# Kernel optimization log

Measured on AMD Instinct MI355X. Metric: run time of the kernel, lower is better.

The kernel has to match this reference:

```python
import jax, jax.numpy as jnp
import numpy as np

N = 65536   # total goals in library
D = 256     # flattened embedding dim
B = 2048    # batch_size (last B entries are the new batch)


def setup_inputs() -> dict:
    key = jax.random.key(0)
    k1, k2 = jax.random.split(key)
    return {
        "target_lib": jax.random.normal(k1, (N, D), dtype=jnp.float32),
        "reached_lib": jax.random.normal(k2, (N, D), dtype=jnp.float32),
        "batch_size": B,
    }


def _euclid(a, b):
    # distance_fn: Euclidean distance between two embeddings
    return jnp.sqrt(jnp.sum((a - b) ** 2))


def _nearest_idx(queries, lib):
    # top-1 nearest neighbor via squared-distance expansion (same argmin as cdist)
    qn = jnp.sum(queries * queries, axis=1, keepdims=True)      # [B,1]
    ln = jnp.sum(lib * lib, axis=1)                             # [L]
    d2 = qn + ln[None, :] - 2.0 * (queries @ lib.T)             # [B,L]
    return jnp.argmin(d2, axis=1)                               # [B]


def reference(target_lib, reached_lib, batch_size):
    targets = target_lib[-batch_size:]          # [B,D] newest target goals
    reached = reached_lib[-batch_size:]         # [B,D] newest reached goals
    prev = reached_lib[:-batch_size]            # [N-B,D] previously reached goals

    prev_closest = prev[_nearest_idx(targets, prev)]       # [B,D]
    new_closest = reached[_nearest_idx(targets, reached)]  # [B,D]

    def LP(t, init_e, reached_e):
        return _euclid(t, init_e) - _euclid(t, reached_e)

    IM_vals, IM_grads = jax.vmap(jax.value_and_grad(LP, 0))(
        targets, prev_closest, new_closest)
    return IM_vals, IM_grads
```

## Files before the change

kernel.cpp:

```cpp
#include <hip/hip_runtime.h>
#include <math.h>

#define NTOT   65536
#define DDIM   256
#define BATCH  2048
#define NPREV  (NTOT - BATCH)

#define PWP    32
#define PWR    32
#define UPC_P  31
#define UPC_R  1
#define BNC_P  31
#define BNC_R  16

#define INF_F 3.402823466e+38f
#define SWZ(r) ((((r) & 3)) ^ ((((r) >> 2) & 3)))

typedef float  f32x4  __attribute__((ext_vector_type(4)));
typedef float  f32x16 __attribute__((ext_vector_type(16)));
typedef _Float16 half8 __attribute__((ext_vector_type(8)));

#define TILE_HALVES 65536

#define SCHED_FENCE() __builtin_amdgcn_sched_barrier(0)
#define RAW_BARRIER() do { SCHED_FENCE(); __builtin_amdgcn_s_barrier(); SCHED_FENCE(); } while (0)
#define VMCNT2()  do { asm volatile("s_waitcnt vmcnt(2)" ::: "memory"); SCHED_FENCE(); } while (0)
#define VMCNT0()  do { asm volatile("s_waitcnt vmcnt(0)" ::: "memory"); SCHED_FENCE(); } while (0)
#define LGKM0()   do { asm volatile("s_waitcnt lgkmcnt(0)" ::: "memory"); SCHED_FENCE(); } while (0)

__global__ void lp_norms(const float* __restrict__ lib, float* __restrict__ ln) {
    const int row  = blockIdx.x * 4 + (threadIdx.x >> 6);
    const int lane = threadIdx.x & 63;
    const float4 v = reinterpret_cast<const float4*>(lib + (size_t)row * DDIM)[lane];
    float s = v.x * v.x + v.y * v.y + v.z * v.z + v.w * v.w;
#pragma unroll
    for (int off = 32; off > 0; off >>= 1) s += __shfl_down(s, off);
    if (lane == 0) ln[row] = s;
}

__device__ __forceinline__ void cvt_split(const f32x4 a, const f32x4 b,
                                          half8& h, half8& l) {
    float v[8] = {a[0], a[1], a[2], a[3], b[0], b[1], b[2], b[3]};
#pragma unroll
    for (int j = 0; j < 8; ++j) {
        const float s = v[j] * 256.0f;
        const _Float16 hh = (_Float16)s;
        const _Float16 ll = (_Float16)(s - (float)hh);
        h[j] = hh; l[j] = ll;
    }
}

__global__ void lp_split32(const float* __restrict__ src, _Float16* __restrict__ dst,
                           float* __restrict__ ln) {
    const int tile = blockIdx.x;
    const int t    = threadIdx.x;
    const int rg   = t >> 6;
    const int l    = t & 63;
    const int row  = rg * 32 + (l & 31);
    const int k8   = l >> 5;
    const float* srcR = src + (size_t)tile * 128 * DDIM + (size_t)row * DDIM;
    _Float16*    dstT = dst + (size_t)tile * TILE_HALVES;

    float nsum = 0.f;
#pragma unroll
    for (int kb = 0; kb < 8; ++kb) {
#pragma unroll
        for (int kk = 0; kk < 2; ++kk) {
            const float* p = srcR + kb * 32 + kk * 16 + k8 * 8;
            const f32x4 a = *reinterpret_cast<const f32x4*>(p);
            const f32x4 b = *reinterpret_cast<const f32x4*>(p + 4);
            half8 h, lo; cvt_split(a, b, h, lo);
            const size_t off = ((size_t)(((kb * 2 + 0) * 4 + rg) * 2 + kk) * 64 + l) * 8;
            *reinterpret_cast<half8*>(dstT + off)        = h;
            *reinterpret_cast<half8*>(dstT + off + 4096) = lo;
            nsum += a[0]*a[0] + a[1]*a[1] + a[2]*a[2] + a[3]*a[3]
                  + b[0]*b[0] + b[1]*b[1] + b[2]*b[2] + b[3]*b[3];
        }
    }
    nsum += __shfl_xor(nsum, 32);
    if (ln != nullptr && k8 == 0) ln[(size_t)tile * 128 + row] = nsum;
}

__device__ __forceinline__ void gload16(const _Float16* g, _Float16* lds) {
    __builtin_amdgcn_global_load_lds(
        (const __attribute__((address_space(1))) void*)g,
        (__attribute__((address_space(3))) void*)lds, 16, 0, 0);
}

#define NN_STEP(kb_, RC, RN, STAGE_OK, VM, READ_OK)                              \
  {                                                                              \
    const int s_ = un * 8 + (kb_);                                               \
    if (STAGE_OK) stageL((s_ + 2) % 3, s_ + 2);                                  \
    VM;                                                                          \
    RAW_BARRIER();                                                               \
    LGKM0();                                                                     \
    __builtin_amdgcn_s_setprio(1);                                               \
    _Pragma("unroll")                                                            \
    for (int kk = 0; kk < 2; ++kk)                                               \
      _Pragma("unroll")                                                          \
      for (int term = 0; term < 3; ++term) {                                     \
        const int ta = (term == 2) ? 1 : 0;                                      \
        const int tb = (term == 1) ? 1 : 0;                                      \
        acc[0] = __builtin_amdgcn_mfma_f32_32x32x16_f16(                         \
            qf[kb_][ta][kk], RC[0][tb][kk], acc[0], 0, 0, 0);                    \
        acc[1] = __builtin_amdgcn_mfma_f32_32x32x16_f16(                         \
            qf[kb_][ta][kk], RC[1][tb][kk], acc[1], 0, 0, 0);                    \
      }                                                                          \
    __builtin_amdgcn_s_setprio(0);                                               \
    if (READ_OK) {                                                               \
      const _Float16* Bn = &LB[(s_ + 1) % 3][0];                                 \
      _Pragma("unroll")                                                          \
      for (int nf = 0; nf < 2; ++nf)                                             \
        _Pragma("unroll")                                                        \
        for (int hl = 0; hl < 2; ++hl)                                           \
          _Pragma("unroll")                                                      \
          for (int kk = 0; kk < 2; ++kk)                                         \
            RN[nf][hl][kk] = *reinterpret_cast<const half8*>(                    \
                Bn + hl * 2048 + nf * 1024 + kk * 512 + lane * 8);               \
    }                                                                            \
  }

__global__ __launch_bounds__(256, 2)
void lp_nn_mfma10(const _Float16* __restrict__ Qs, const _Float16* __restrict__ Ls,
                  const float* __restrict__ ln, int unitsPC, int nchunks,
                  float* __restrict__ pscore, int* __restrict__ pidx)
{
    __shared__ _Float16 LB[3][4096];
    __shared__ float lnLds[2048];

    const int nwg  = 16 * nchunks;
    const int hid  = blockIdx.x;
    const int work = (hid & 7) * (nwg >> 3) + (hid >> 3);
    const int bx   = work & 15;
    const int by   = work >> 4;

    const int t    = threadIdx.x;
    const int lane = t & 63;
    const int wid  = t >> 6;
    const int col  = lane & 31, hi = lane >> 5;

    const _Float16* Qt = Qs + (size_t)bx * TILE_HALVES;
    const int u0    = by * unitsPC;
    const int NSTEP = unitsPC * 8;

    half8 qf[8][2][2];
#pragma unroll
    for (int kb = 0; kb < 8; ++kb)
#pragma unroll
        for (int hl = 0; hl < 2; ++hl)
#pragma unroll
            for (int kk = 0; kk < 2; ++kk)
                qf[kb][hl][kk] = *reinterpret_cast<const half8*>(
                    Qt + ((((kb * 2 + hl) * 4 + wid) * 2) + kk) * 512 + lane * 8);

    auto stageL = [&](int buf, int s) {
        const int u = u0 + (s >> 3), kb = s & 7;
        const int tile = u >> 1, half = u & 1;
        const _Float16* base = Ls + (size_t)tile * TILE_HALVES;
#pragma unroll
        for (int hl = 0; hl < 2; ++hl)
            gload16(base + ((kb * 2 + hl) * 4 + half * 2) * 1024 + t * 8,
                    &LB[buf][hl * 2048 + wid * 512]);
    };

    float bkey[16];
    int   bidxr[16];
    f32x16 acc[2];
#pragma unroll
    for (int r = 0; r < 16; ++r) { bkey[r] = INF_F; bidxr[r] = 0x7fffffff; }
    acc[0] = (f32x16)(0.f); acc[1] = (f32x16)(0.f);

    auto fold = [&](int un) {
        const int u = u0 + un;
        const float lnv0 = lnLds[un * 64 + col];
        const float lnv1 = lnLds[un * 64 + 32 + col];
#pragma unroll
        for (int nf = 0; nf < 2; ++nf) {
            const int gidx = u * 64 + nf * 32 + col;
            const float lnvs = (nf ? lnv1 : lnv0) * 65536.0f;
#pragma unroll
            for (int r = 0; r < 16; ++r) {
                const float key = fmaf(-2.f, acc[nf][r], lnvs);
                if (key < bkey[r] || (key == bkey[r] && gidx < bidxr[r])) {
                    bkey[r] = key; bidxr[r] = gidx;
                }
                acc[nf][r] = 0.f;
            }
        }
    };

    {
        const float* lsrc = ln + (size_t)u0 * 64;
#pragma unroll
        for (int j = 0; j < 2; ++j)
            __builtin_amdgcn_global_load_lds(
                (const __attribute__((address_space(1))) void*)(lsrc + j * 1024 + t * 4),
                (__attribute__((address_space(3))) void*)(&lnLds[j * 1024 + wid * 256]),
                16, 0, 0);
    }
    stageL(0, 0);
    stageL(1, 1);
    VMCNT2();
    RAW_BARRIER();

    half8 bfA[2][2][2], bfB[2][2][2];
#pragma unroll
    for (int nf = 0; nf < 2; ++nf)
#pragma unroll
        for (int hl = 0; hl < 2; ++hl)
#pragma unroll
            for (int kk = 0; kk < 2; ++kk)
                bfA[nf][hl][kk] = *reinterpret_cast<const half8*>(
                    &LB[0][0] + hl * 2048 + nf * 1024 + kk * 512 + lane * 8);

    for (int un = 0; un < unitsPC - 1; ++un) {
        NN_STEP(0, bfA, bfB, true, VMCNT2(), true)
        NN_STEP(1, bfB, bfA, true, VMCNT2(), true)
        NN_STEP(2, bfA, bfB, true, VMCNT2(), true)
        NN_STEP(3, bfB, bfA, true, VMCNT2(), true)
        NN_STEP(4, bfA, bfB, true, VMCNT2(), true)
        NN_STEP(5, bfB, bfA, true, VMCNT2(), true)
        NN_STEP(6, bfA, bfB, true, VMCNT2(), true)
        NN_STEP(7, bfB, bfA, true, VMCNT2(), true)
        fold(un);
    }
    {
        const int un = unitsPC - 1;
        NN_STEP(0, bfA, bfB, true,  VMCNT2(), true)
        NN_STEP(1, bfB, bfA, true,  VMCNT2(), true)
        NN_STEP(2, bfA, bfB, true,  VMCNT2(), true)
        NN_STEP(3, bfB, bfA, true,  VMCNT2(), true)
        NN_STEP(4, bfA, bfB, true,  VMCNT2(), true)
        NN_STEP(5, bfB, bfA, true,  VMCNT2(), true)
        NN_STEP(6, bfA, bfB, false, VMCNT0(), true)
        NN_STEP(7, bfB, bfA, false, VMCNT0(), false)
        fold(un);
    }

#pragma unroll
    for (int off = 1; off < 32; off <<= 1)
#pragma unroll
        for (int r = 0; r < 16; ++r) {
            const float ok = __shfl_xor(bkey[r], off);
            const int   oi = __shfl_xor(bidxr[r], off);
            if (ok < bkey[r] || (ok == bkey[r] && oi < bidxr[r])) {
                bkey[r] = ok; bidxr[r] = oi;
            }
        }
    if (col == 0)
#pragma unroll
        for (int r = 0; r < 16; ++r) {
            const int q = bx * 128 + wid * 32 + (r & 3) + 8 * (r >> 2) + 4 * hi;
            pscore[(size_t)q * nchunks + by] = bkey[r];
            pidx  [(size_t)q * nchunks + by] = bidxr[r];
        }
}

__global__ __launch_bounds__(256, 2)
void lp_nn_mfma_fb(const float* __restrict__ Q, const float* __restrict__ L,
                   const float* __restrict__ ln, int chunkRows,
                   float* __restrict__ pscore, int* __restrict__ pidx, int nchunks)
{
    __shared__ _Float16 Ah[128 * 32];
    __shared__ _Float16 Al[128 * 32];
    __shared__ _Float16 Bh[128 * 32];
    __shared__ _Float16 Bl[128 * 32];
    __shared__ float xk[2][128];
    __shared__ int   xi[2][128];

    const int t    = threadIdx.x;
    const int wid  = t >> 6, lane = t & 63;
    const int wq   = wid >> 1, wl = wid & 1;
    const int col  = lane & 15, rg = lane >> 4;
    const int qbase = blockIdx.x * 128;
    const int chunkBase = blockIdx.y * chunkRows;
    const int srow   = t >> 2;
    const int schunk = t & 3;

    float bkey[4][4];
    int   bidxr[4][4];
#pragma unroll
    for (int mf = 0; mf < 4; ++mf)
#pragma unroll
        for (int i = 0; i < 4; ++i) { bkey[mf][i] = INF_F; bidxr[mf][i] = 0x7fffffff; }

    for (int lt = 0; lt < chunkRows; lt += 128) {
        f32x4 acc[4][4];
#pragma unroll
        for (int mf = 0; mf < 4; ++mf)
#pragma unroll
            for (int nf = 0; nf < 4; ++nf) acc[mf][nf] = (f32x4)(0.f);

        for (int kb = 0; kb < DDIM; kb += 32) {
            __syncthreads();
#pragma unroll
            for (int sr = 0; sr < 2; ++sr) {
                const int r = srow + 64 * sr;
                const int s = schunk ^ SWZ(r);
                {
                    const float* src = Q + (size_t)(qbase + r) * DDIM + kb + schunk * 8;
                    const f32x4 a = *reinterpret_cast<const f32x4*>(src);
                    const f32x4 b = *reinterpret_cast<const f32x4*>(src + 4);
                    half8 h, l; cvt_split(a, b, h, l);
                    *reinterpret_cast<half8*>(&Ah[r * 32 + s * 8]) = h;
                    *reinterpret_cast<half8*>(&Al[r * 32 + s * 8]) = l;
                }
                {
                    const float* src = L + (size_t)(chunkBase + lt + r) * DDIM + kb + schunk * 8;
                    const f32x4 a = *reinterpret_cast<const f32x4*>(src);
                    const f32x4 b = *reinterpret_cast<const f32x4*>(src + 4);
                    half8 h, l; cvt_split(a, b, h, l);
                    *reinterpret_cast<half8*>(&Bh[r * 32 + s * 8]) = h;
                    *reinterpret_cast<half8*>(&Bl[r * 32 + s * 8]) = l;
                }
            }
            __syncthreads();

            half8 ah[4], al[4];
#pragma unroll
            for (int mf = 0; mf < 4; ++mf) {
                const int r = wq * 64 + mf * 16 + col;
                const int s = rg ^ SWZ(r);
                ah[mf] = *reinterpret_cast<const half8*>(&Ah[r * 32 + s * 8]);
                al[mf] = *reinterpret_cast<const half8*>(&Al[r * 32 + s * 8]);
            }
#pragma unroll
            for (int nf = 0; nf < 4; ++nf) {
                const int r = wl * 64 + nf * 16 + col;
                const int s = rg ^ SWZ(r);
                const half8 bh = *reinterpret_cast<const half8*>(&Bh[r * 32 + s * 8]);
                const half8 bl = *reinterpret_cast<const half8*>(&Bl[r * 32 + s * 8]);
#pragma unroll
                for (int mf = 0; mf < 4; ++mf) {
                    acc[mf][nf] = __builtin_amdgcn_mfma_f32_16x16x32_f16(ah[mf], bh, acc[mf][nf], 0, 0, 0);
                    acc[mf][nf] = __builtin_amdgcn_mfma_f32_16x16x32_f16(ah[mf], bl, acc[mf][nf], 0, 0, 0);
                    acc[mf][nf] = __builtin_amdgcn_mfma_f32_16x16x32_f16(al[mf], bh, acc[mf][nf], 0, 0, 0);
                }
            }
        }

#pragma unroll
        for (int nf = 0; nf < 4; ++nf) {
            const int gidx = chunkBase + lt + wl * 64 + nf * 16 + col;
            const float lnv = ln[gidx] * 65536.0f;
#pragma unroll
            for (int mf = 0; mf < 4; ++mf)
#pragma unroll
                for (int i = 0; i < 4; ++i) {
                    const float key = fmaf(-2.f, acc[mf][nf][i], lnv);
                    if (key < bkey[mf][i] || (key == bkey[mf][i] && gidx < bidxr[mf][i])) {
                        bkey[mf][i] = key; bidxr[mf][i] = gidx;
                    }
                }
        }
    }

#pragma unroll
    for (int off = 1; off < 16; off <<= 1)
#pragma unroll
        for (int mf = 0; mf < 4; ++mf)
#pragma unroll
            for (int i = 0; i < 4; ++i) {
                const float ok = __shfl_xor(bkey[mf][i], off);
                const int   oi = __shfl_xor(bidxr[mf][i], off);
                if (ok < bkey[mf][i] || (ok == bkey[mf][i] && oi < bidxr[mf][i])) {
                    bkey[mf][i] = ok; bidxr[mf][i] = oi;
                }
            }
    if (col == 0)
#pragma unroll
        for (int mf = 0; mf < 4; ++mf)
#pragma unroll
            for (int i = 0; i < 4; ++i) {
                const int ql = wq * 64 + mf * 16 + rg * 4 + i;
                xk[wl][ql] = bkey[mf][i];
                xi[wl][ql] = bidxr[mf][i];
            }
    __syncthreads();
    if (t < 128) {
        float bk = xk[0][t]; int bi = xi[0][t];
        const float k2 = xk[1][t]; const int i2 = xi[1][t];
        if (k2 < bk || (k2 == bk && i2 < bi)) { bk = k2; bi = i2; }
        const int q = qbase + t;
        pscore[(size_t)q * nchunks + blockIdx.y] = bk;
        pidx  [(size_t)q * nchunks + blockIdx.y] = bi;
    }
}

__global__ void lp_finalize(const float* __restrict__ Q,
                            const float* __restrict__ prevL,
                            const float* __restrict__ reachL,
                            const float* __restrict__ ps_p, const int* __restrict__ pi_p,
                            const float* __restrict__ ps_r, const int* __restrict__ pi_r,
                            int ncp, int ncr,
                            float* __restrict__ out)
{
    const int q = blockIdx.x;
    const int lane = threadIdx.x;

    float k1 = (lane < ncp) ? ps_p[(size_t)q * ncp + lane] : INF_F;
    int   i1 = (lane < ncp) ? pi_p[(size_t)q * ncp + lane] : 0x7fffffff;
#pragma unroll
    for (int off = 32; off > 0; off >>= 1) {
        const float ok = __shfl_xor(k1, off);
        const int   oi = __shfl_xor(i1, off);
        if (ok < k1 || (ok == k1 && oi < i1)) { k1 = ok; i1 = oi; }
    }
    float k2 = (lane < ncr) ? ps_r[(size_t)q * ncr + lane] : INF_F;
    int   i2 = (lane < ncr) ? pi_r[(size_t)q * ncr + lane] : 0x7fffffff;
#pragma unroll
    for (int off = 32; off > 0; off >>= 1) {
        const float ok = __shfl_xor(k2, off);
        const int   oi = __shfl_xor(i2, off);
        if (ok < k2 || (ok == k2 && oi < i2)) { k2 = ok; i2 = oi; }
    }

    const float4 tv = reinterpret_cast<const float4*>(Q      + (size_t)q  * DDIM)[lane];
    const float4 e1 = reinterpret_cast<const float4*>(prevL  + (size_t)i1 * DDIM)[lane];
    const float4 e2 = reinterpret_cast<const float4*>(reachL + (size_t)i2 * DDIM)[lane];
    const float4 d1 = {tv.x - e1.x, tv.y - e1.y, tv.z - e1.z, tv.w - e1.w};
    const float4 d2 = {tv.x - e2.x, tv.y - e2.y, tv.z - e2.z, tv.w - e2.w};
    float s1 = d1.x * d1.x + d1.y * d1.y + d1.z * d1.z + d1.w * d1.w;
    float s2 = d2.x * d2.x + d2.y * d2.y + d2.z * d2.z + d2.w * d2.w;
#pragma unroll
    for (int off = 32; off > 0; off >>= 1) {
        s1 += __shfl_xor(s1, off);
        s2 += __shfl_xor(s2, off);
    }
    const float r1 = sqrtf(s1), r2 = sqrtf(s2);
    float4 g;
    g.x = d1.x / r1 - d2.x / r2;
    g.y = d1.y / r1 - d2.y / r2;
    g.z = d1.z / r1 - d2.z / r2;
    g.w = d1.w / r1 - d2.w / r2;
    reinterpret_cast<float4*>(out + BATCH + (size_t)q * DDIM)[lane] = g;
    if (lane == 0) out[q] = r1 - r2;
}

extern "C" void kernel_launch(void* const* d_in, const int* in_sizes, int n_in,
                              void* d_out, int out_size, void* d_ws, size_t ws_size,
                              hipStream_t stream) {
    const float* target_lib  = (const float*)d_in[0];
    const float* reached_lib = (const float*)d_in[1];
    const float* Qp     = target_lib  + (size_t)NPREV * DDIM;
    const float* prevL  = reached_lib;
    const float* reachL = reached_lib + (size_t)NPREV * DDIM;

    float* ws     = (float*)d_ws;
    float* ln_all = ws;
    float* ps_p   = ln_all + NTOT;
    float* ps_r   = ps_p + (size_t)BATCH * PWP;
    int*   pi_p   = (int*)(ps_r + (size_t)BATCH * PWR);
    int*   pi_r   = pi_p + (size_t)BATCH * PWP;
    _Float16* Qsp = (_Float16*)(pi_r + (size_t)BATCH * PWR);
    _Float16* Lsp = Qsp + (size_t)(BATCH / 128) * TILE_HALVES;
    float* out    = (float*)d_out;

    const size_t need = (size_t)(NTOT + 2 * BATCH * (PWP + PWR)) * 4
                      + (size_t)(BATCH / 128 + NTOT / 128) * TILE_HALVES * 2;

    if (ws_size >= need) {
        lp_split32<<<NTOT / 128, 256, 0, stream>>>(reached_lib, Lsp, ln_all);
        lp_split32<<<BATCH / 128, 256, 0, stream>>>(Qp, Qsp, nullptr);
        lp_nn_mfma10<<<16 * PWP, 256, 0, stream>>>(
            Qsp, Lsp, ln_all, UPC_P, PWP, ps_p, pi_p);
        lp_nn_mfma10<<<16 * PWR, 256, 0, stream>>>(
            Qsp, Lsp + (size_t)(NPREV / 128) * TILE_HALVES,
            ln_all + NPREV, UPC_R, PWR, ps_r, pi_r);
        lp_finalize<<<BATCH, 64, 0, stream>>>(
            Qp, prevL, reachL, ps_p, pi_p, ps_r, pi_r, PWP, PWR, out);
    } else {
        lp_norms<<<NTOT / 4, 256, 0, stream>>>(reached_lib, ln_all);
        lp_nn_mfma_fb<<<dim3(BATCH / 128, BNC_P), 256, 0, stream>>>(
            Qp, prevL, ln_all, 2048, ps_p, pi_p, BNC_P);
        lp_nn_mfma_fb<<<dim3(BATCH / 128, BNC_R), 256, 0, stream>>>(
            Qp, reachL, ln_all + NPREV, 128, ps_r, pi_r, BNC_R);
        lp_finalize<<<BATCH, 64, 0, stream>>>(
            Qp, prevL, reachL, ps_p, pi_p, ps_r, pi_r, BNC_P, BNC_R, out);
    }
}
```

Before: 237.0 us.

## Stage two k-blocks per LDS buffer to halve barriers in NN MFMA loop

The nearest-neighbour MFMA kernel now stages two k-blocks of library fragments per triple-buffered LDS slot, with the LDS buffers doubled to match. Each pair of k-steps shares one wait and one barrier, and the next pair's loads are issued between the two MFMA groups. The aim is to halve the per-step barrier and waitcnt overhead. In exchange, each iteration waits for all outstanding global loads (vmcnt(0)), including the prefetch that was just issued. That shortens the effective prefetch distance and could expose memory latency. LDS use per block also grows.

```diff
diff --git a/kernel.cpp b/kernel.cpp
--- a/kernel.cpp
+++ b/kernel.cpp
@@ -24,7 +24,7 @@
 
 #define SCHED_FENCE() __builtin_amdgcn_sched_barrier(0)
 #define RAW_BARRIER() do { SCHED_FENCE(); __builtin_amdgcn_s_barrier(); SCHED_FENCE(); } while (0)
-#define VMCNT2()  do { asm volatile("s_waitcnt vmcnt(2)" ::: "memory"); SCHED_FENCE(); } while (0)
+#define VMCNT4()  do { asm volatile("s_waitcnt vmcnt(4)" ::: "memory"); SCHED_FENCE(); } while (0)
 #define VMCNT0()  do { asm volatile("s_waitcnt vmcnt(0)" ::: "memory"); SCHED_FENCE(); } while (0)
 #define LGKM0()   do { asm volatile("s_waitcnt lgkmcnt(0)" ::: "memory"); SCHED_FENCE(); } while (0)
 
@@ -87,14 +87,17 @@
         (__attribute__((address_space(3))) void*)lds, 16, 0, 0);
 }
 
-#define NN_STEP(kb_, RC, RN, STAGE_OK, VM, READ_OK)                              \
-  {                                                                              \
-    const int s_ = un * 8 + (kb_);                                               \
-    if (STAGE_OK) stageL((s_ + 2) % 3, s_ + 2);                                  \
-    VM;                                                                          \
-    RAW_BARRIER();                                                               \
-    LGKM0();                                                                     \
-    __builtin_amdgcn_s_setprio(1);                                               \
+#define READ8(R, BASE)                                                           \
+    _Pragma("unroll")                                                            \
+    for (int nf = 0; nf < 2; ++nf)                                               \
+      _Pragma("unroll")                                                          \
+      for (int hl = 0; hl < 2; ++hl)                                             \
+        _Pragma("unroll")                                                        \
+        for (int kk = 0; kk < 2; ++kk)                                           \
+          R[nf][hl][kk] = *reinterpret_cast<const half8*>(                       \
+              (BASE) + hl * 2048 + nf * 1024 + kk * 512 + lane * 8);
+
+#define MFMA12(kb_, RC)                                                          \
     _Pragma("unroll")                                                            \
     for (int kk = 0; kk < 2; ++kk)                                               \
       _Pragma("unroll")                                                          \
@@ -105,27 +108,33 @@
             qf[kb_][ta][kk], RC[0][tb][kk], acc[0], 0, 0, 0);                    \
         acc[1] = __builtin_amdgcn_mfma_f32_32x32x16_f16(                         \
             qf[kb_][ta][kk], RC[1][tb][kk], acc[1], 0, 0, 0);                    \
-      }                                                                          \
+      }
+
+#define NN_PAIR(j_, STAGE_OK, FOLD_OK)                                           \
+  {                                                                              \
+    const int p_ = un * 4 + (j_);                                                \
+    VMCNT0();                     \
+    RAW_BARRIER();                                                               \
+    LGKM0();                        \
+    __builtin_amdgcn_s_setprio(1);                                               \
+    MFMA12(2 * (j_), bfE)                                                        \
     __builtin_amdgcn_s_setprio(0);                                               \
-    if (READ_OK) {                                                               \
-      const _Float16* Bn = &LB[(s_ + 1) % 3][0];                                 \
-      _Pragma("unroll")                                                          \
-      for (int nf = 0; nf < 2; ++nf)                                             \
-        _Pragma("unroll")                                                        \
-        for (int hl = 0; hl < 2; ++hl)                                           \
-          _Pragma("unroll")                                                      \
-          for (int kk = 0; kk < 2; ++kk)                                         \
-            RN[nf][hl][kk] = *reinterpret_cast<const half8*>(                    \
-                Bn + hl * 2048 + nf * 1024 + kk * 512 + lane * 8);               \
-    }                                                                            \
+    { const _Float16* Bc = &LB[p_ % 3][4096]; READ8(bfO, Bc) }                    \
+    LGKM0();                                                                     \
+    if (STAGE_OK) stageP((p_ + 2) % 3, p_ + 2);                                  \
+    __builtin_amdgcn_s_setprio(1);                                               \
+    MFMA12(2 * (j_) + 1, bfO)                                                    \
+    __builtin_amdgcn_s_setprio(0);                                               \
+    { const _Float16* Bn = &LB[(p_ + 1) % 3][0]; READ8(bfE, Bn) }                 \
+    if (FOLD_OK) fold(un);                                                       \
   }
 
 __global__ __launch_bounds__(256, 2)
-void lp_nn_mfma10(const _Float16* __restrict__ Qs, const _Float16* __restrict__ Ls,
+void lp_nn_mfma11(const _Float16* __restrict__ Qs, const _Float16* __restrict__ Ls,
                   const float* __restrict__ ln, int unitsPC, int nchunks,
                   float* __restrict__ pscore, int* __restrict__ pidx)
 {
-    __shared__ _Float16 LB[3][4096];
+    __shared__ _Float16 LB[3][8192];
     __shared__ float lnLds[2048];
 
     const int nwg  = 16 * nchunks;
@@ -140,8 +149,7 @@
     const int col  = lane & 31, hi = lane >> 5;
 
     const _Float16* Qt = Qs + (size_t)bx * TILE_HALVES;
-    const int u0    = by * unitsPC;
-    const int NSTEP = unitsPC * 8;
+    const int u0 = by * unitsPC;
 
     half8 qf[8][2][2];
 #pragma unroll
@@ -153,14 +161,16 @@
                 qf[kb][hl][kk] = *reinterpret_cast<const half8*>(
                     Qt + ((((kb * 2 + hl) * 4 + wid) * 2) + kk) * 512 + lane * 8);
 
-    auto stageL = [&](int buf, int s) {
-        const int u = u0 + (s >> 3), kb = s & 7;
+    auto stageP = [&](int buf, int p) {
+        const int u = u0 + (p >> 2), kb0 = (p & 3) * 2;
         const int tile = u >> 1, half = u & 1;
         const _Float16* base = Ls + (size_t)tile * TILE_HALVES;
 #pragma unroll
-        for (int hl = 0; hl < 2; ++hl)
-            gload16(base + ((kb * 2 + hl) * 4 + half * 2) * 1024 + t * 8,
-                    &LB[buf][hl * 2048 + wid * 512]);
+        for (int dkb = 0; dkb < 2; ++dkb)
+#pragma unroll
+            for (int hl = 0; hl < 2; ++hl)
+                gload16(base + (((kb0 + dkb) * 2 + hl) * 4 + half * 2) * 1024 + t * 8,
+                        &LB[buf][(dkb * 2 + hl) * 2048 + wid * 512]);
     };
 
     float bkey[16];
@@ -198,43 +208,26 @@
                 (__attribute__((address_space(3))) void*)(&lnLds[j * 1024 + wid * 256]),
                 16, 0, 0);
     }
-    stageL(0, 0);
-    stageL(1, 1);
-    VMCNT2();
+    stageP(0, 0);
+    stageP(1, 1);
+    VMCNT4();
     RAW_BARRIER();
 
-    half8 bfA[2][2][2], bfB[2][2][2];
-#pragma unroll
-    for (int nf = 0; nf < 2; ++nf)
-#pragma unroll
-        for (int hl = 0; hl < 2; ++hl)
-#pragma unroll
-            for (int kk = 0; kk < 2; ++kk)
-                bfA[nf][hl][kk] = *reinterpret_cast<const half8*>(
-                    &LB[0][0] + hl * 2048 + nf * 1024 + kk * 512 + lane * 8);
+    half8 bfE[2][2][2], bfO[2][2][2];
+    { const _Float16* B0 = &LB[0][0]; READ8(bfE, B0) }
 
     for (int un = 0; un < unitsPC - 1; ++un) {
-        NN_STEP(0, bfA, bfB, true, VMCNT2(), true)
-        NN_STEP(1, bfB, bfA, true, VMCNT2(), true)
-        NN_STEP(2, bfA, bfB, true, VMCNT2(), true)
-        NN_STEP(3, bfB, bfA, true, VMCNT2(), true)
-        NN_STEP(4, bfA, bfB, true, VMCNT2(), true)
-        NN_STEP(5, bfB, bfA, true, VMCNT2(), true)
-        NN_STEP(6, bfA, bfB, true, VMCNT2(), true)
-        NN_STEP(7, bfB, bfA, true, VMCNT2(), true)
-        fold(un);
+        NN_PAIR(0, true, false)
+        NN_PAIR(1, true, false)
+        NN_PAIR(2, true, false)
+        NN_PAIR(3, true, true)
     }
     {
         const int un = unitsPC - 1;
-        NN_STEP(0, bfA, bfB, true,  VMCNT2(), true)
-        NN_STEP(1, bfB, bfA, true,  VMCNT2(), true)
-        NN_STEP(2, bfA, bfB, true,  VMCNT2(), true)
-        NN_STEP(3, bfB, bfA, true,  VMCNT2(), true)
-        NN_STEP(4, bfA, bfB, true,  VMCNT2(), true)
-        NN_STEP(5, bfB, bfA, true,  VMCNT2(), true)
-        NN_STEP(6, bfA, bfB, false, VMCNT0(), true)
-        NN_STEP(7, bfB, bfA, false, VMCNT0(), false)
-        fold(un);
+        NN_PAIR(0, true,  false)
+        NN_PAIR(1, true,  false)
+        NN_PAIR(2, false, false)
+        NN_PAIR(3, false, true)
     }
 
 #pragma unroll
@@ -462,9 +455,9 @@
     if (ws_size >= need) {
         lp_split32<<<NTOT / 128, 256, 0, stream>>>(reached_lib, Lsp, ln_all);
         lp_split32<<<BATCH / 128, 256, 0, stream>>>(Qp, Qsp, nullptr);
-        lp_nn_mfma10<<<16 * PWP, 256, 0, stream>>>(
+        lp_nn_mfma11<<<16 * PWP, 256, 0, stream>>>(
             Qsp, Lsp, ln_all, UPC_P, PWP, ps_p, pi_p);
-        lp_nn_mfma10<<<16 * PWR, 256, 0, stream>>>(
+        lp_nn_mfma11<<<16 * PWR, 256, 0, stream>>>(
             Qsp, Lsp + (size_t)(NPREV / 128) * TILE_HALVES,
             ln_all + NPREV, UPC_R, PWR, ps_r, pi_r);
         lp_finalize<<<BATCH, 64, 0, stream>>>(
```

Result: no change. 240.5 us (+1.5%).
